# Optimization experiments

Measured on AMD Instinct MI355X. Metric: run time of the kernel, lower is better.

The kernel has to match this reference:

```python
import jax, jax.numpy as jnp
import numpy as np

D_MODEL = 1024
N_HEADS = 16
HEAD_DIM = D_MODEL // N_HEADS


def setup_inputs() -> dict:
    key = jax.random.key(0)
    ks = jax.random.split(key, 11)
    B, S = 2, 2048
    s = 1.0 / np.sqrt(D_MODEL)
    return {
        "query": jax.random.normal(ks[0], (B, S, D_MODEL), jnp.float32),
        "key": jax.random.normal(ks[1], (B, S, D_MODEL), jnp.float32),
        "value": jax.random.normal(ks[2], (B, S, D_MODEL), jnp.float32),
        "Wq": jax.random.normal(ks[3], (D_MODEL, D_MODEL), jnp.float32) * s,
        "bq": jnp.zeros((D_MODEL,), jnp.float32),
        "Wk": jax.random.normal(ks[4], (D_MODEL, D_MODEL), jnp.float32) * s,
        "bk": jnp.zeros((D_MODEL,), jnp.float32),
        "Wv": jax.random.normal(ks[5], (D_MODEL, D_MODEL), jnp.float32) * s,
        "bv": jnp.zeros((D_MODEL,), jnp.float32),
        "Wo": jax.random.normal(ks[6], (D_MODEL, D_MODEL), jnp.float32) * s,
        "bo": jnp.zeros((D_MODEL,), jnp.float32),
    }


def reference(query, key, value, Wq, bq, Wk, bk, Wv, bv, Wo, bo):
    B, S, _ = query.shape
    H, Dh = N_HEADS, HEAD_DIM
    scale = jnp.sqrt(jnp.asarray(Dh, query.dtype))
    # projections (torch Linear: x @ W.T + b)
    Q = (query @ Wq.T + bq).reshape(B, S, H, Dh).transpose(0, 2, 1, 3)  # [B,H,S,Dh]
    K = (key @ Wk.T + bk).reshape(B, S, H, Dh).transpose(0, 2, 1, 3)
    V = (value @ Wv.T + bv).reshape(B, S, H, Dh).transpose(0, 2, 1, 3)
    # full score matrix, matching the naive formulation
    energy = jnp.einsum("bhqd,bhkd->bhqk", Q, K) / scale  # [B,H,S,S]
    attn = jax.nn.softmax(energy, axis=-1)
    # dropout: eval mode -> identity
    out = jnp.einsum("bhqk,bhkd->bhqd", attn, V)  # [B,H,S,Dh]
    out = out.transpose(0, 2, 1, 3).reshape(B, S, H * Dh)
    return out @ Wo.T + bo
```

## Files before the change

### kernel.cpp

```cpp
#include <hip/hip_runtime.h>
#include <hip/hip_bf16.h>
#include <stdint.h>


typedef unsigned short u16;
typedef __attribute__((ext_vector_type(8))) short bf16x8;
typedef __attribute__((ext_vector_type(4))) float f32x4;

#define MFMA16 __builtin_amdgcn_mfma_f32_16x16x32_bf16
#define AS1 __attribute__((address_space(1)))
#define AS3 __attribute__((address_space(3)))

#define GM 4096
#define GN 1024
#define GK 1024
#define S_LEN 2048
#define NH 16
#define DH 64
#define KVBLK 64
#define PSTR 72
#define TILE_ELEMS (128 * 64)
#define HT_ELEMS  (128 * 64)
#define SLOT_ELEMS (256 * 64)

__device__ __forceinline__ u16 f2bf(float f) {
    union { float f; uint32_t u; } v; v.f = f;
    return (u16)((v.u + 0x7fffu + ((v.u >> 16) & 1u)) >> 16);
}

__device__ __forceinline__ uint32_t pack_bf16(float lo, float hi) {
    float2 t; t.x = lo; t.y = hi;
    __hip_bfloat162 h = __float22bfloat162_rn(t);
    return *(uint32_t*)&h;
}

__global__ __launch_bounds__(256) void cvt_all_kernel(
        const float* __restrict__ q, const float* __restrict__ k, const float* __restrict__ v,
        const float* __restrict__ Wq, const float* __restrict__ Wk,
        const float* __restrict__ Wv, const float* __restrict__ Wo,
        const float* __restrict__ bq,
        u16* __restrict__ qbf, u16* __restrict__ kbf, u16* __restrict__ vbf,
        u16* __restrict__ Wqb, u16* __restrict__ Wkb, u16* __restrict__ Wvb,
        u16* __restrict__ Wob, float* __restrict__ bqs, float qscale) {
    int bid = blockIdx.x;
    if (bid >= 8192) {
        int i = (bid - 8192) * 256 + (int)threadIdx.x;
        if (i < GN) bqs[i] = bq[i] * qscale;
        return;
    }
    const float* src; u16* dst; float scale = 1.f; int off;
    if      (bid < 2048) { src = q;  dst = qbf; off = bid; }
    else if (bid < 4096) { src = k;  dst = kbf; off = bid - 2048; }
    else if (bid < 6144) { src = v;  dst = vbf; off = bid - 4096; }
    else if (bid < 6656) { src = Wq; dst = Wqb; off = bid - 6144; scale = qscale; }
    else if (bid < 7168) { src = Wk; dst = Wkb; off = bid - 6656; }
    else if (bid < 7680) { src = Wv; dst = Wvb; off = bid - 7168; }
    else                 { src = Wo; dst = Wob; off = bid - 7680; }
    size_t i = (size_t)off * 256 + threadIdx.x;
    const f32x4* s = (const f32x4*)src + i * 2;
    f32x4 a = s[0], b = s[1];
    union { bf16x8 v8; u16 u[8]; } o;
    o.u[0] = f2bf(a[0] * scale); o.u[1] = f2bf(a[1] * scale);
    o.u[2] = f2bf(a[2] * scale); o.u[3] = f2bf(a[3] * scale);
    o.u[4] = f2bf(b[0] * scale); o.u[5] = f2bf(b[1] * scale);
    o.u[6] = f2bf(b[2] * scale); o.u[7] = f2bf(b[3] * scale);
    *(bf16x8*)(dst + i * 8) = o.v8;
}

__device__ __forceinline__ void gemm256_core(const u16* __restrict__ A,
                                             const u16* __restrict__ W,
                                             const float* __restrict__ bias,
                                             u16* __restrict__ Cout, int mode,
                                             u16* As, u16* Bs,
                                             int mbase, int nbase) {
    const int t  = threadIdx.x;
    const int l  = t & 63;
    const int w  = t >> 6;
    const int wr = w >> 2, wc = w & 3;
    const int cl = l & 15, g = l >> 4;
    const int wcH = wc >> 1;

    f32x4 acc[8][4];
    f32x4 zero = {0.f, 0.f, 0.f, 0.f};
    #pragma unroll
    for (int i = 0; i < 8; ++i)
        #pragma unroll
        for (int j = 0; j < 4; ++j) acc[i][j] = zero;

    #define STAGE_HALF(Tarr, gptr, gbase, s, h, kt)                                        \
        do {                                                                               \
            _Pragma("unroll")                                                              \
            for (int qq = 0; qq < 2; ++qq) {                                               \
                int c = qq * 512 + t;                                                      \
                int row = c >> 3;                                                          \
                int c8 = (c & 7) ^ (row & 7);                                              \
                __builtin_amdgcn_global_load_lds(                                          \
                    (const AS1 void*)(gptr + (size_t)((gbase) + (h) * 128 + row) * GK + (kt) + c8 * 8), \
                    (AS3 void*)(Tarr + (s) * SLOT_ELEMS + (h) * HT_ELEMS + c * 8), 16, 0, 0); \
            }                                                                              \
        } while (0)

    STAGE_HALF(As, A, mbase, 0, 0, 0); STAGE_HALF(As, A, mbase, 0, 1, 0);
    STAGE_HALF(Bs, W, nbase, 0, 0, 0); STAGE_HALF(Bs, W, nbase, 0, 1, 0);
    asm volatile("s_waitcnt vmcnt(0)" ::: "memory");
    __builtin_amdgcn_s_barrier();

    const int NK = GK / 64;
    for (int i = 0; i < NK; ++i) {
        const int slot = i & 1;
        const u16* Asb = As + slot * SLOT_ELEMS + wr * HT_ELEMS;
        const u16* Bsb = Bs + slot * SLOT_ELEMS + wcH * HT_ELEMS;
        const int nkt = (i + 1) * 64;
        const bool pre = (i + 1 < NK);

        #pragma unroll
        for (int p = 0; p < 4; ++p) {
            if (pre) {
                if (p == 0) STAGE_HALF(As, A, mbase, slot ^ 1, 0, nkt);
                if (p == 1) STAGE_HALF(As, A, mbase, slot ^ 1, 1, nkt);
                if (p == 2) STAGE_HALF(Bs, W, nbase, slot ^ 1, 0, nkt);
                if (p == 3) STAGE_HALF(Bs, W, nbase, slot ^ 1, 1, nkt);
            }
            const int mh = p & 1, ks = p >> 1;
            bf16x8 af[4], bfr[4];
            #pragma unroll
            for (int mi = 0; mi < 4; ++mi) {
                int r = (mh * 4 + mi) * 16 + cl;
                af[mi] = *(const bf16x8*)&Asb[r * 64 + ((ks * 4 + g) ^ (r & 7)) * 8];
            }
            #pragma unroll
            for (int nj = 0; nj < 4; ++nj) {
                int r = (wc & 1) * 64 + nj * 16 + cl;
                bfr[nj] = *(const bf16x8*)&Bsb[r * 64 + ((ks * 4 + g) ^ (r & 7)) * 8];
            }
            __builtin_amdgcn_s_setprio(1);
            #pragma unroll
            for (int mi = 0; mi < 4; ++mi)
                #pragma unroll
                for (int nj = 0; nj < 4; ++nj)
                    acc[mh * 4 + mi][nj] =
                        MFMA16(af[mi], bfr[nj], acc[mh * 4 + mi][nj], 0, 0, 0);
            __builtin_amdgcn_s_setprio(0);
            if (p < 3) __builtin_amdgcn_s_barrier();
        }
        if (pre) {
            asm volatile("s_waitcnt vmcnt(0)" ::: "memory");
            __builtin_amdgcn_s_barrier();
        }
    }
    #undef STAGE_HALF

    #pragma unroll
    for (int mi = 0; mi < 8; ++mi) {
        #pragma unroll
        for (int nj = 0; nj < 4; ++nj) {
            int n = nbase + wc * 64 + nj * 16 + cl;
            float bv = bias[n];
            #pragma unroll
            for (int r = 0; r < 4; ++r) {
                int m = mbase + wr * 128 + mi * 16 + g * 4 + r;
                float vv = acc[mi][nj][r] + bv;
                int b = m >> 11, s = m & 2047;
                int h = n >> 6, dh = n & 63;
                if (mode == 0)
                    Cout[(((size_t)(b * NH + h)) * S_LEN + s) * DH + dh] = f2bf(vv);
                else
                    Cout[(((size_t)(b * NH + h)) * DH + dh) * S_LEN + s] = f2bf(vv);
            }
        }
    }
}

__global__ __launch_bounds__(512, 2) void proj_gemm(
        const u16* __restrict__ qbf, const u16* __restrict__ kbf, const u16* __restrict__ vbf,
        const u16* __restrict__ Wqb, const u16* __restrict__ Wkb, const u16* __restrict__ Wvb,
        const float* __restrict__ bq, const float* __restrict__ bk, const float* __restrict__ bv,
        u16* __restrict__ Qb, u16* __restrict__ Kb, u16* __restrict__ Vtb) {
    __shared__ u16 As[2 * SLOT_ELEMS];
    __shared__ u16 Bs[2 * SLOT_ELEMS];
    int bid = blockIdx.x;
    int lid = (bid & 7) * 24 + (bid >> 3);
    int x = lid & 3;
    int y = (lid >> 2) & 15;
    int z = lid >> 6;
    const u16* A   = (z == 0) ? qbf : (z == 1) ? kbf : vbf;
    const u16* W   = (z == 0) ? Wqb : (z == 1) ? Wkb : Wvb;
    const float* b = (z == 0) ? bq  : (z == 1) ? bk  : bv;
    u16* C         = (z == 0) ? Qb  : (z == 1) ? Kb  : Vtb;
    gemm256_core(A, W, b, C, (z == 2) ? 1 : 0, As, Bs, y * 256, x * 256);
}

__device__ __forceinline__ void gemm_core(const u16* __restrict__ A,
                                          const u16* __restrict__ W,
                                          const float* __restrict__ bias,
                                          float* __restrict__ Cout,
                                          u16* As, u16* Bs,
                                          int mbase, int nbase) {
    const int t  = threadIdx.x;
    const int l  = t & 63;
    const int w  = t >> 6;
    const int wr = w >> 1, wc = w & 1;
    const int cl = l & 15, g = l >> 4;
    const int rx = cl & 7;

    f32x4 acc[4][4];
    f32x4 zero = {0.f, 0.f, 0.f, 0.f};
    #pragma unroll
    for (int i = 0; i < 4; ++i)
        #pragma unroll
        for (int j = 0; j < 4; ++j) acc[i][j] = zero;

    #define GSTAGE(buf, kt)                                                                 \
        do {                                                                                \
            _Pragma("unroll")                                                               \
            for (int r = 0; r < 4; ++r) {                                                   \
                int c = r * 256 + t;                                                        \
                int row = c >> 3;                                                           \
                int c8 = (c & 7) ^ (row & 7);                                               \
                __builtin_amdgcn_global_load_lds(                                           \
                    (const AS1 void*)(A + (size_t)(mbase + row) * GK + (kt) + c8 * 8),      \
                    (AS3 void*)(As + (buf) * TILE_ELEMS + c * 8), 16, 0, 0);                \
                __builtin_amdgcn_global_load_lds(                                           \
                    (const AS1 void*)(W + (size_t)(nbase + row) * GK + (kt) + c8 * 8),      \
                    (AS3 void*)(Bs + (buf) * TILE_ELEMS + c * 8), 16, 0, 0);                \
            }                                                                               \
        } while (0)

    GSTAGE(0, 0);
    __syncthreads();

    int cur = 0;
    for (int kt = 0; kt < GK; kt += 64) {
        if (kt + 64 < GK) GSTAGE(cur ^ 1, kt + 64);

        const u16* Asb = As + cur * TILE_ELEMS;
        const u16* Bsb = Bs + cur * TILE_ELEMS;
        #pragma unroll
        for (int ks = 0; ks < 2; ++ks) {
            bf16x8 af[4], bfr[4];
            #pragma unroll
            for (int mi = 0; mi < 4; ++mi) {
                int row = wr * 64 + mi * 16 + cl;
                af[mi] = *(const bf16x8*)&Asb[row * 64 + ((ks * 4 + g) ^ rx) * 8];
            }
            #pragma unroll
            for (int nj = 0; nj < 4; ++nj) {
                int row = wc * 64 + nj * 16 + cl;
                bfr[nj] = *(const bf16x8*)&Bsb[row * 64 + ((ks * 4 + g) ^ rx) * 8];
            }
            #pragma unroll
            for (int mi = 0; mi < 4; ++mi)
                #pragma unroll
                for (int nj = 0; nj < 4; ++nj)
                    acc[mi][nj] = MFMA16(af[mi], bfr[nj], acc[mi][nj], 0, 0, 0);
        }
        __syncthreads();
        cur ^= 1;
    }
    #undef GSTAGE

    #pragma unroll
    for (int mi = 0; mi < 4; ++mi) {
        #pragma unroll
        for (int nj = 0; nj < 4; ++nj) {
            int n = nbase + wc * 64 + nj * 16 + cl;
            float bv = bias[n];
            #pragma unroll
            for (int r = 0; r < 4; ++r) {
                int m = mbase + wr * 64 + mi * 16 + g * 4 + r;
                Cout[(size_t)m * GN + n] = acc[mi][nj][r] + bv;
            }
        }
    }
}

__global__ __launch_bounds__(256) void out_gemm(const u16* __restrict__ A,
                                                const u16* __restrict__ W,
                                                const float* __restrict__ bias,
                                                float* __restrict__ C) {
    __shared__ u16 As[2 * TILE_ELEMS];
    __shared__ u16 Bs[2 * TILE_ELEMS];
    int bid = blockIdx.x;
    int lid = (bid & 7) * 32 + (bid >> 3);
    int x = lid & 7, y = lid >> 3;
    gemm_core(A, W, bias, C, As, Bs, y * 128, x * 128);
}

__global__ __launch_bounds__(512, 4) void attn_kernel(const u16* __restrict__ Q,
                                                      const u16* __restrict__ Kb,
                                                      const u16* __restrict__ Vt,
                                                      u16* __restrict__ O) {
    __shared__ u16 Ks[3][KVBLK * 64];
    __shared__ u16 Vs[3][KVBLK * 64];
    __shared__ u16 Pl[8][16 * PSTR];

    const int t = threadIdx.x, l = t & 63, w = t >> 6;
    const int cl = l & 15, g = l >> 4;
    const int bh = blockIdx.x;
    const int b = bh >> 4, h = bh & 15;
    const int qw = blockIdx.y * 128 + w * 16;

    const u16* Qp = Q  + ((size_t)bh * S_LEN + qw) * DH;
    const u16* Kp = Kb + (size_t)bh * S_LEN * DH;
    const u16* Vp = Vt + (size_t)bh * DH * S_LEN;

    bf16x8 qf0 = *(const bf16x8*)(Qp + (size_t)cl * DH + g * 8);
    bf16x8 qf1 = *(const bf16x8*)(Qp + (size_t)cl * DH + 32 + g * 8);

    float rs = 0.f;
    f32x4 oacc[4];
    f32x4 zero = {0.f, 0.f, 0.f, 0.f};
    #pragma unroll
    for (int tt = 0; tt < 4; ++tt) oacc[tt] = zero;

    u16* P = Pl[w];

    const int srow = t >> 3;
    const int sc8  = (t & 7) ^ (srow & 7);
    const u16* Kg = Kp + (size_t)srow * DH + sc8 * 8;
    const u16* Vg = Vp + (size_t)srow * S_LEN + sc8 * 8;

    #define STAGE(buf, kvoff)                                                            \
        do {                                                                             \
            __builtin_amdgcn_global_load_lds(                                            \
                (const AS1 void*)(Kg + (size_t)(kvoff) * DH),                            \
                (AS3 void*)(&Ks[buf][0] + t * 8), 16, 0, 0);                             \
            __builtin_amdgcn_global_load_lds(                                            \
                (const AS1 void*)(Vg + (kvoff)),                                         \
                (AS3 void*)(&Vs[buf][0] + t * 8), 16, 0, 0);                             \
        } while (0)

    STAGE(0, 0);
    STAGE(1, KVBLK);
    asm volatile("s_waitcnt vmcnt(2)" ::: "memory");
    __builtin_amdgcn_s_barrier();

    const int NT = S_LEN / KVBLK;
    int cur = 0;
    for (int it = 0; it < NT; ++it) {
        if (it + 2 < NT) {
            int nb = cur + 2; if (nb >= 3) nb -= 3;
            STAGE(nb, (it + 2) * KVBLK);
        }

        const u16* Ksb = &Ks[cur][0];
        const u16* Vsb = &Vs[cur][0];

        f32x4 s[4];
        #pragma unroll
        for (int j = 0; j < 4; ++j) s[j] = zero;
        __builtin_amdgcn_s_setprio(1);
        #pragma unroll
        for (int j = 0; j < 4; ++j) {
            int row = j * 16 + cl, rx = row & 7;
            bf16x8 k0 = *(const bf16x8*)&Ksb[row * 64 + ((g)     ^ rx) * 8];
            bf16x8 k1 = *(const bf16x8*)&Ksb[row * 64 + ((4 + g) ^ rx) * 8];
            s[j] = MFMA16(k0, qf0, s[j], 0, 0, 0);
            s[j] = MFMA16(k1, qf1, s[j], 0, 0, 0);
        }
        __builtin_amdgcn_s_setprio(0);

        #pragma unroll
        for (int j = 0; j < 4; ++j) {
            float p0 = __builtin_amdgcn_exp2f(s[j][0]);
            float p1 = __builtin_amdgcn_exp2f(s[j][1]);
            float p2 = __builtin_amdgcn_exp2f(s[j][2]);
            float p3 = __builtin_amdgcn_exp2f(s[j][3]);
            rs += (p0 + p1) + (p2 + p3);
            uint2 pk;
            pk.x = pack_bf16(p0, p1);
            pk.y = pack_bf16(p2, p3);
            *(uint2*)&P[cl * PSTR + j * 16 + g * 4] = pk;
        }

        bf16x8 pf[2];
        #pragma unroll
        for (int ks = 0; ks < 2; ++ks)
            pf[ks] = *(const bf16x8*)&P[cl * PSTR + ks * 32 + g * 8];

        __builtin_amdgcn_s_setprio(1);
        #pragma unroll
        for (int tt = 0; tt < 4; ++tt) {
            int row = tt * 16 + cl, rx = row & 7;
            #pragma unroll
            for (int ks = 0; ks < 2; ++ks) {
                bf16x8 vf = *(const bf16x8*)&Vsb[row * 64 + ((ks * 4 + g) ^ rx) * 8];
                oacc[tt] = MFMA16(pf[ks], vf, oacc[tt], 0, 0, 0);
            }
        }
        __builtin_amdgcn_s_setprio(0);

        if (it + 2 < NT) {
            asm volatile("s_waitcnt vmcnt(2)\n\ts_barrier" ::: "memory");
        } else {
            asm volatile("s_waitcnt vmcnt(0)\n\ts_barrier" ::: "memory");
        }
        cur = (cur + 1 == 3) ? 0 : cur + 1;
    }
    #undef STAGE

    rs += __shfl_xor(rs, 16, 64);
    rs += __shfl_xor(rs, 32, 64);
    float rsq[4];
    #pragma unroll
    for (int r = 0; r < 4; ++r)
        rsq[r] = __shfl(rs, g * 4 + r, 64);

    #pragma unroll
    for (int tt = 0; tt < 4; ++tt) {
        #pragma unroll
        for (int r = 0; r < 4; ++r) {
            int q = qw + g * 4 + r;
            float val = oacc[tt][r] / rsq[r];
            O[((size_t)b * S_LEN + q) * GN + h * DH + tt * 16 + cl] = f2bf(val);
        }
    }
}

extern "C" void kernel_launch(void* const* d_in, const int* in_sizes, int n_in,
                              void* d_out, int out_size, void* d_ws, size_t ws_size,
                              hipStream_t stream) {
    const float* query = (const float*)d_in[0];
    const float* key   = (const float*)d_in[1];
    const float* value = (const float*)d_in[2];
    const float* Wq = (const float*)d_in[3];
    const float* bq = (const float*)d_in[4];
    const float* Wk = (const float*)d_in[5];
    const float* bk = (const float*)d_in[6];
    const float* Wv = (const float*)d_in[7];
    const float* bv = (const float*)d_in[8];
    const float* Wo = (const float*)d_in[9];
    const float* bo = (const float*)d_in[10];
    float* out = (float*)d_out;

    const float QSCALE = 0.125f * 1.4426950408889634f;

    u16* ws = (u16*)d_ws;
    const size_t MD = (size_t)GM * GN;
    const size_t WW = (size_t)GN * GK;
    u16* qbf = ws;
    u16* kbf = qbf + MD;
    u16* vbf = kbf + MD;
    u16* Wqb = vbf + MD;
    u16* Wkb = Wqb + WW;
    u16* Wvb = Wkb + WW;
    u16* Wob = Wvb + WW;
    u16* Qb  = Wob + WW;
    u16* Kbf = Qb  + MD;
    u16* Vtb = Kbf + MD;
    u16* Ob  = Vtb + MD;
    float* bqs = (float*)(Ob + MD);

    cvt_all_kernel<<<8196, 256, 0, stream>>>(query, key, value, Wq, Wk, Wv, Wo, bq,
                                             qbf, kbf, vbf, Wqb, Wkb, Wvb, Wob,
                                             bqs, QSCALE);

    proj_gemm<<<192, 512, 0, stream>>>(qbf, kbf, vbf, Wqb, Wkb, Wvb,
                                       bqs, bk, bv, Qb, Kbf, Vtb);

    dim3 gattn(2 * NH, S_LEN / 128);
    attn_kernel<<<gattn, 512, 0, stream>>>(Qb, Kbf, Vtb, Ob);

    out_gemm<<<256, 256, 0, stream>>>(Ob, Wob, bo, out);
}
```

Baseline: 154.7 us.

## Fuse fp32-to-bf16 activation conversion into projection GEMM A-tile loading

Activation conversion of query/key/value moves out of the separate conversion kernel. The projection GEMM now loads fp32 activations into registers, packs them to bf16 and stores them to LDS, while weights still stream through global_load_lds. This removes the write and re-read of three bf16 activation buffers. The GEMM also shrinks from 256x256 tiles with 512 threads to 128x128 tiles with 256 threads, drops the setprio/phased barrier scheme, and launches a 3D grid of 768 blocks. In exchange, A traffic into the GEMM doubles in bytes, and conversion ALU work plus register staging now sit on the critical loop.

Result: no change. 156.3 us (+1.1%).

```diff
diff --git a/kernel.cpp b/kernel.cpp
--- a/kernel.cpp
+++ b/kernel.cpp
@@ -20,8 +20,6 @@
 #define KVBLK 64
 #define PSTR 72
 #define TILE_ELEMS (128 * 64)
-#define HT_ELEMS  (128 * 64)
-#define SLOT_ELEMS (256 * 64)
 
 __device__ __forceinline__ u16 f2bf(float f) {
     union { float f; uint32_t u; } v; v.f = f;
@@ -34,28 +32,23 @@
     return *(uint32_t*)&h;
 }
 
-__global__ __launch_bounds__(256) void cvt_all_kernel(
-        const float* __restrict__ q, const float* __restrict__ k, const float* __restrict__ v,
+__global__ __launch_bounds__(256) void cvt_w_kernel(
         const float* __restrict__ Wq, const float* __restrict__ Wk,
         const float* __restrict__ Wv, const float* __restrict__ Wo,
         const float* __restrict__ bq,
-        u16* __restrict__ qbf, u16* __restrict__ kbf, u16* __restrict__ vbf,
         u16* __restrict__ Wqb, u16* __restrict__ Wkb, u16* __restrict__ Wvb,
         u16* __restrict__ Wob, float* __restrict__ bqs, float qscale) {
     int bid = blockIdx.x;
-    if (bid >= 8192) {
-        int i = (bid - 8192) * 256 + (int)threadIdx.x;
+    if (bid >= 2048) {
+        int i = (bid - 2048) * 256 + (int)threadIdx.x;
         if (i < GN) bqs[i] = bq[i] * qscale;
         return;
     }
     const float* src; u16* dst; float scale = 1.f; int off;
-    if      (bid < 2048) { src = q;  dst = qbf; off = bid; }
-    else if (bid < 4096) { src = k;  dst = kbf; off = bid - 2048; }
-    else if (bid < 6144) { src = v;  dst = vbf; off = bid - 4096; }
-    else if (bid < 6656) { src = Wq; dst = Wqb; off = bid - 6144; scale = qscale; }
-    else if (bid < 7168) { src = Wk; dst = Wkb; off = bid - 6656; }
-    else if (bid < 7680) { src = Wv; dst = Wvb; off = bid - 7168; }
-    else                 { src = Wo; dst = Wob; off = bid - 7680; }
+    if      (bid < 512)  { src = Wq; dst = Wqb; off = bid;        scale = qscale; }
+    else if (bid < 1024) { src = Wk; dst = Wkb; off = bid - 512;  }
+    else if (bid < 1536) { src = Wv; dst = Wvb; off = bid - 1024; }
+    else                 { src = Wo; dst = Wob; off = bid - 1536; }
     size_t i = (size_t)off * 256 + threadIdx.x;
     const f32x4* s = (const f32x4*)src + i * 2;
     f32x4 a = s[0], b = s[1];
@@ -67,98 +60,121 @@
     *(bf16x8*)(dst + i * 8) = o.v8;
 }
 
-__device__ __forceinline__ void gemm256_core(const u16* __restrict__ A,
-                                             const u16* __restrict__ W,
-                                             const float* __restrict__ bias,
-                                             u16* __restrict__ Cout, int mode,
-                                             u16* As, u16* Bs,
-                                             int mbase, int nbase) {
+__device__ __forceinline__ void proj_core(const float* __restrict__ Af,
+                                          const u16* __restrict__ W,
+                                          const float* __restrict__ bias,
+                                          u16* __restrict__ Cout, int mode,
+                                          u16* As, u16* Bs,
+                                          int mbase, int nbase) {
     const int t  = threadIdx.x;
     const int l  = t & 63;
     const int w  = t >> 6;
-    const int wr = w >> 2, wc = w & 3;
+    const int wr = w >> 1, wc = w & 1;
     const int cl = l & 15, g = l >> 4;
-    const int wcH = wc >> 1;
-
-    f32x4 acc[8][4];
+    const int rx = cl & 7;
+
+    f32x4 acc[4][4];
     f32x4 zero = {0.f, 0.f, 0.f, 0.f};
     #pragma unroll
-    for (int i = 0; i < 8; ++i)
+    for (int i = 0; i < 4; ++i)
         #pragma unroll
         for (int j = 0; j < 4; ++j) acc[i][j] = zero;
 
-    #define STAGE_HALF(Tarr, gptr, gbase, s, h, kt)                                        \
-        do {                                                                               \
-            _Pragma("unroll")                                                              \
-            for (int qq = 0; qq < 2; ++qq) {                                               \
-                int c = qq * 512 + t;                                                      \
-                int row = c >> 3;                                                          \
-                int c8 = (c & 7) ^ (row & 7);                                              \
-                __builtin_amdgcn_global_load_lds(                                          \
-                    (const AS1 void*)(gptr + (size_t)((gbase) + (h) * 128 + row) * GK + (kt) + c8 * 8), \
-                    (AS3 void*)(Tarr + (s) * SLOT_ELEMS + (h) * HT_ELEMS + c * 8), 16, 0, 0); \
-            }                                                                              \
+    const float* Aaddr[4];
+    const u16*  Waddr[4];
+    #pragma unroll
+    for (int r = 0; r < 4; ++r) {
+        int c = r * 256 + t;
+        int row = c >> 3;
+        int c8 = (c & 7) ^ (row & 7);
+        Aaddr[r] = Af + (size_t)(mbase + row) * GK + c8 * 8;
+        Waddr[r] = W  + (size_t)(nbase + row) * GK + c8 * 8;
+    }
+
+    f32x4 ar[4][2];
+
+    #define LOAD_A(kt)                                                        \
+        do {                                                                  \
+            _Pragma("unroll")                                                 \
+            for (int r = 0; r < 4; ++r) {                                     \
+                ar[r][0] = *(const f32x4*)(Aaddr[r] + (kt));                  \
+                ar[r][1] = *(const f32x4*)(Aaddr[r] + (kt) + 4);              \
+            }                                                                 \
         } while (0)
 
-    STAGE_HALF(As, A, mbase, 0, 0, 0); STAGE_HALF(As, A, mbase, 0, 1, 0);
-    STAGE_HALF(Bs, W, nbase, 0, 0, 0); STAGE_HALF(Bs, W, nbase, 0, 1, 0);
-    asm volatile("s_waitcnt vmcnt(0)" ::: "memory");
-    __builtin_amdgcn_s_barrier();
-
-    const int NK = GK / 64;
-    for (int i = 0; i < NK; ++i) {
-        const int slot = i & 1;
-        const u16* Asb = As + slot * SLOT_ELEMS + wr * HT_ELEMS;
-        const u16* Bsb = Bs + slot * SLOT_ELEMS + wcH * HT_ELEMS;
-        const int nkt = (i + 1) * 64;
-        const bool pre = (i + 1 < NK);
-
-        #pragma unroll
-        for (int p = 0; p < 4; ++p) {
-            if (pre) {
-                if (p == 0) STAGE_HALF(As, A, mbase, slot ^ 1, 0, nkt);
-                if (p == 1) STAGE_HALF(As, A, mbase, slot ^ 1, 1, nkt);
-                if (p == 2) STAGE_HALF(Bs, W, nbase, slot ^ 1, 0, nkt);
-                if (p == 3) STAGE_HALF(Bs, W, nbase, slot ^ 1, 1, nkt);
-            }
-            const int mh = p & 1, ks = p >> 1;
+    #define STORE_A(buf)                                                      \
+        do {                                                                  \
+            _Pragma("unroll")                                                 \
+            for (int r = 0; r < 4; ++r) {                                     \
+                int c = r * 256 + t;                                          \
+                union { bf16x8 v8; uint32_t u[4]; } o;                        \
+                o.u[0] = pack_bf16(ar[r][0][0], ar[r][0][1]);                 \
+                o.u[1] = pack_bf16(ar[r][0][2], ar[r][0][3]);                 \
+                o.u[2] = pack_bf16(ar[r][1][0], ar[r][1][1]);                 \
+                o.u[3] = pack_bf16(ar[r][1][2], ar[r][1][3]);                 \
+                *(bf16x8*)&As[(buf) * TILE_ELEMS + c * 8] = o.v8;             \
+            }                                                                 \
+        } while (0)
+
+    #define STAGE_B(buf, kt)                                                  \
+        do {                                                                  \
+            _Pragma("unroll")                                                 \
+            for (int r = 0; r < 4; ++r) {                                     \
+                int c = r * 256 + t;                                          \
+                __builtin_amdgcn_global_load_lds(                             \
+                    (const AS1 void*)(Waddr[r] + (kt)),                       \
+                    (AS3 void*)(Bs + (buf) * TILE_ELEMS + c * 8), 16, 0, 0);  \
+            }                                                                 \
+        } while (0)
+
+    LOAD_A(0);
+    STAGE_B(0, 0);
+    STORE_A(0);
+    __syncthreads();
+
+    int cur = 0;
+    for (int kt = 0; kt < GK; kt += 64) {
+        const bool pre = (kt + 64 < GK);
+        if (pre) { LOAD_A(kt + 64); STAGE_B(cur ^ 1, kt + 64); }
+
+        const u16* Asb = As + cur * TILE_ELEMS;
+        const u16* Bsb = Bs + cur * TILE_ELEMS;
+        #pragma unroll
+        for (int ks = 0; ks < 2; ++ks) {
             bf16x8 af[4], bfr[4];
             #pragma unroll
             for (int mi = 0; mi < 4; ++mi) {
-                int r = (mh * 4 + mi) * 16 + cl;
-                af[mi] = *(const bf16x8*)&Asb[r * 64 + ((ks * 4 + g) ^ (r & 7)) * 8];
+                int row = wr * 64 + mi * 16 + cl;
+                af[mi] = *(const bf16x8*)&Asb[row * 64 + ((ks * 4 + g) ^ rx) * 8];
             }
             #pragma unroll
             for (int nj = 0; nj < 4; ++nj) {
-                int r = (wc & 1) * 64 + nj * 16 + cl;
-                bfr[nj] = *(const bf16x8*)&Bsb[r * 64 + ((ks * 4 + g) ^ (r & 7)) * 8];
-            }
-            __builtin_amdgcn_s_setprio(1);
+                int row = wc * 64 + nj * 16 + cl;
+                bfr[nj] = *(const bf16x8*)&Bsb[row * 64 + ((ks * 4 + g) ^ rx) * 8];
+            }
             #pragma unroll
             for (int mi = 0; mi < 4; ++mi)
                 #pragma unroll
                 for (int nj = 0; nj < 4; ++nj)
-                    acc[mh * 4 + mi][nj] =
-                        MFMA16(af[mi], bfr[nj], acc[mh * 4 + mi][nj], 0, 0, 0);
-            __builtin_amdgcn_s_setprio(0);
-            if (p < 3) __builtin_amdgcn_s_barrier();
-        }
-        if (pre) {
-            asm volatile("s_waitcnt vmcnt(0)" ::: "memory");
-            __builtin_amdgcn_s_barrier();
-        }
-    }
-    #undef STAGE_HALF
-
-    #pragma unroll
-    for (int mi = 0; mi < 8; ++mi) {
+                    acc[mi][nj] = MFMA16(af[mi], bfr[nj], acc[mi][nj], 0, 0, 0);
+        }
+        if (pre) STORE_A(cur ^ 1);
+        __syncthreads();
+        cur ^= 1;
+    }
+    #undef LOAD_A
+    #undef STORE_A
+    #undef STAGE_B
+
+    #pragma unroll
+    for (int mi = 0; mi < 4; ++mi) {
         #pragma unroll
         for (int nj = 0; nj < 4; ++nj) {
             int n = nbase + wc * 64 + nj * 16 + cl;
             float bv = bias[n];
             #pragma unroll
             for (int r = 0; r < 4; ++r) {
-                int m = mbase + wr * 128 + mi * 16 + g * 4 + r;
+                int m = mbase + wr * 64 + mi * 16 + g * 4 + r;
                 float vv = acc[mi][nj][r] + bv;
                 int b = m >> 11, s = m & 2047;
                 int h = n >> 6, dh = n & 63;
@@ -171,23 +187,21 @@
     }
 }
 
-__global__ __launch_bounds__(512, 2) void proj_gemm(
-        const u16* __restrict__ qbf, const u16* __restrict__ kbf, const u16* __restrict__ vbf,
+__global__ __launch_bounds__(256) void proj_gemm(
+        const float* __restrict__ query, const float* __restrict__ key,
+        const float* __restrict__ value,
         const u16* __restrict__ Wqb, const u16* __restrict__ Wkb, const u16* __restrict__ Wvb,
         const float* __restrict__ bq, const float* __restrict__ bk, const float* __restrict__ bv,
         u16* __restrict__ Qb, u16* __restrict__ Kb, u16* __restrict__ Vtb) {
-    __shared__ u16 As[2 * SLOT_ELEMS];
-    __shared__ u16 Bs[2 * SLOT_ELEMS];
-    int bid = blockIdx.x;
-    int lid = (bid & 7) * 24 + (bid >> 3);
-    int x = lid & 3;
-    int y = (lid >> 2) & 15;
-    int z = lid >> 6;
-    const u16* A   = (z == 0) ? qbf : (z == 1) ? kbf : vbf;
+    __shared__ u16 As[2 * TILE_ELEMS];
+    __shared__ u16 Bs[2 * TILE_ELEMS];
+    int z = blockIdx.z;
+    const float* A = (z == 0) ? query : (z == 1) ? key : value;
     const u16* W   = (z == 0) ? Wqb : (z == 1) ? Wkb : Wvb;
     const float* b = (z == 0) ? bq  : (z == 1) ? bk  : bv;
     u16* C         = (z == 0) ? Qb  : (z == 1) ? Kb  : Vtb;
-    gemm256_core(A, W, b, C, (z == 2) ? 1 : 0, As, Bs, y * 256, x * 256);
+    proj_core(A, W, b, C, (z == 2) ? 1 : 0, As, Bs,
+              blockIdx.y * 128, blockIdx.x * 128);
 }
 
 __device__ __forceinline__ void gemm_core(const u16* __restrict__ A,
@@ -438,10 +452,7 @@
     u16* ws = (u16*)d_ws;
     const size_t MD = (size_t)GM * GN;
     const size_t WW = (size_t)GN * GK;
-    u16* qbf = ws;
-    u16* kbf = qbf + MD;
-    u16* vbf = kbf + MD;
-    u16* Wqb = vbf + MD;
+    u16* Wqb = ws;
     u16* Wkb = Wqb + WW;
     u16* Wvb = Wkb + WW;
     u16* Wob = Wvb + WW;
@@ -451,12 +462,12 @@
     u16* Ob  = Vtb + MD;
     float* bqs = (float*)(Ob + MD);
 
-    cvt_all_kernel<<<8196, 256, 0, stream>>>(query, key, value, Wq, Wk, Wv, Wo, bq,
-                                             qbf, kbf, vbf, Wqb, Wkb, Wvb, Wob,
-                                             bqs, QSCALE);
-
-    proj_gemm<<<192, 512, 0, stream>>>(qbf, kbf, vbf, Wqb, Wkb, Wvb,
-                                       bqs, bk, bv, Qb, Kbf, Vtb);
+    cvt_w_kernel<<<2049, 256, 0, stream>>>(Wq, Wk, Wv, Wo, bq,
+                                           Wqb, Wkb, Wvb, Wob, bqs, QSCALE);
+
+    dim3 gproj(GN / 128, GM / 128, 3);
+    proj_gemm<<<gproj, 256, 0, stream>>>(query, key, value, Wqb, Wkb, Wvb,
+                                         bqs, bk, bv, Qb, Kbf, Vtb);
 
     dim3 gattn(2 * NH, S_LEN / 128);
     attn_kernel<<<gattn, 512, 0, stream>>>(Qb, Kbf, Vtb, Ob);
```
